# Kernel optimization log

Measured on AMD Instinct MI355X. Metric: run time of the kernel, lower is better.

Reference implementation:

```python
import jax, jax.numpy as jnp
import numpy as np

B, S, D = 2, 2048, 1024
H = 16
HEAD_DIM = 64          # matches head_dim init arg; D // H == 64
HALF_WINDOW = 32       # local_window_size // 2
SCALE = HEAD_DIM ** -0.5


def setup_inputs() -> dict:
    key = jax.random.key(0)
    ks = jax.random.split(key, 6)
    std = 1.0 / np.sqrt(D)
    return {
        "x": jax.random.normal(ks[0], (B, S, D), dtype=jnp.float32),
        "Wq": jax.random.normal(ks[1], (D, D), dtype=jnp.float32) * std,
        "Wk": jax.random.normal(ks[2], (D, D), dtype=jnp.float32) * std,
        "Wv": jax.random.normal(ks[3], (D, D), dtype=jnp.float32) * std,
        "Wo": jax.random.normal(ks[4], (D, D), dtype=jnp.float32) * std,
        "bo": jnp.zeros((D,), dtype=jnp.float32),
    }


def reference(x, Wq, Wk, Wv, Wo, bo):
    b, s, d = x.shape
    h, hd = H, d // H

    def split_heads(y):  # [b, s, d] -> [b, h, s, hd]
        return y.reshape(b, s, h, hd).transpose(0, 2, 1, 3)

    q = split_heads(x @ Wq) * SCALE
    k = split_heads(x @ Wk)
    v = split_heads(x @ Wv)

    # dense scores [b, h, s, s] (module materializes full O(S^2) matrix)
    scores = jnp.einsum("bhqd,bhkd->bhqk", q, k)

    # local window |i-j| <= HALF_WINDOW combined with causal j <= i
    i = jnp.arange(s)
    local = jnp.abs(i[:, None] - i[None, :]) <= HALF_WINDOW
    causal = i[None, :] <= i[:, None]
    mask = local & causal  # [s, s]
    scores = jnp.where(mask[None, None, :, :], scores, -jnp.inf)

    attn = jax.nn.softmax(scores, axis=-1)  # diagonal always valid -> no NaN
    out = jnp.einsum("bhqk,bhkd->bhqd", attn, v)
    out = out.transpose(0, 2, 1, 3).reshape(b, s, d)  # merge heads
    return out @ Wo + bo
```

## Files before the change

### kernel.cpp

```cpp
#include <hip/hip_runtime.h>
#include <hip/hip_bf16.h>

typedef __bf16 bf16_t;
typedef __bf16 bf16x8 __attribute__((ext_vector_type(8)));
typedef __bf16 bf16x4 __attribute__((ext_vector_type(4)));
typedef float  f32x4  __attribute__((ext_vector_type(4)));

#define B_   2
#define S_   2048
#define D_   1024
#define H_   16
#define HD_  64
#define HW   32
#define SCALE_ 0.125f

__device__ __forceinline__ void gl_lds16(const bf16_t* g, bf16_t* l) {
  __builtin_amdgcn_global_load_lds(
      (const __attribute__((address_space(1))) void*)g,
      (__attribute__((address_space(3))) void*)l, 16, 0, 0);
}

__global__ __launch_bounds__(256) void k_conv(const float* __restrict__ X,
                                              const float* __restrict__ W0,
                                              const float* __restrict__ W1,
                                              const float* __restrict__ W2,
                                              const float* __restrict__ W3,
                                              bf16_t* __restrict__ Xb,
                                              bf16_t* __restrict__ Wt) {
  __shared__ bf16_t t[64][72];
  int bid = blockIdx.x;
  int tid = threadIdx.x;
  if (bid < 2048) {
    int i = bid * 256 + tid;
    const float4 a = ((const float4*)X)[i * 2];
    const float4 b = ((const float4*)X)[i * 2 + 1];
    bf16x8 r;
    r[0] = (bf16_t)a.x; r[1] = (bf16_t)a.y; r[2] = (bf16_t)a.z; r[3] = (bf16_t)a.w;
    r[4] = (bf16_t)b.x; r[5] = (bf16_t)b.y; r[6] = (bf16_t)b.z; r[7] = (bf16_t)b.w;
    ((bf16x8*)Xb)[i] = r;
    return;
  }
  int wb = bid - 2048;
  int wsel = wb >> 8;
  const float* W = (wsel == 0) ? W0 : (wsel == 1) ? W1 : (wsel == 2) ? W2 : W3;
  bf16_t* dst = Wt + (size_t)wsel * D_ * D_;
  int tile = wb & 255;
  int k0 = (tile >> 4) * 64, n0 = (tile & 15) * 64;
  int r = tid >> 4, c4 = (tid & 15) * 4;
#pragma unroll
  for (int i = 0; i < 4; ++i) {
    int row = i * 16 + r;
    float4 v = *(const float4*)(W + (size_t)(k0 + row) * D_ + n0 + c4);
    t[row][c4 + 0] = (bf16_t)v.x;
    t[row][c4 + 1] = (bf16_t)v.y;
    t[row][c4 + 2] = (bf16_t)v.z;
    t[row][c4 + 3] = (bf16_t)v.w;
  }
  __syncthreads();
#pragma unroll
  for (int i = 0; i < 4; ++i) {
    int row = i * 16 + r;
    bf16x4 o;
    o[0] = t[c4 + 0][row];
    o[1] = t[c4 + 1][row];
    o[2] = t[c4 + 2][row];
    o[3] = t[c4 + 3][row];
    *(bf16x4*)(dst + (size_t)(n0 + row) * D_ + k0 + c4) = o;
  }
}

__global__ __launch_bounds__(256) void k_gemm_qkv(const bf16_t* __restrict__ X,
                                                  const bf16_t* __restrict__ Wt,
                                                  bf16_t* __restrict__ Q,
                                                  bf16_t* __restrict__ K,
                                                  bf16_t* __restrict__ V) {
  __shared__ bf16_t sA[128 * 32];
  __shared__ bf16_t sB[128 * 32];
  int bid = blockIdx.x;
  int xcd = bid & 7, idx = bid >> 3;
  int mt = ((xcd & 3) << 3) + (idx & 7);
  int nt = (xcd >> 2) * 12 + (idx >> 3);
  int wsel = nt >> 3;
  int n0 = (nt & 7) * 128, m0 = mt * 128;
  const bf16_t* Wp = Wt + (size_t)wsel * D_ * D_;
  int tid = threadIdx.x, lane = tid & 63, wave = tid >> 6;
  int wr = (wave >> 1) * 64, wc = (wave & 1) * 64;
  int r0 = wave * 32 + (lane >> 2);
  int ce = (lane & 3) * 8;
  const bf16_t* gA0 = X + (size_t)(m0 + r0) * D_ + ce;
  const bf16_t* gB0 = Wp + (size_t)(n0 + r0) * D_ + ce;
  bf16_t* lA0 = sA + wave * 1024;
  bf16_t* lB0 = sB + wave * 1024;
  f32x4 acc[4][4] = {};
  int kq = (lane >> 4) * 8, rl = lane & 15;
  for (int kt = 0; kt < D_; kt += 32) {
    __syncthreads();
    gl_lds16(gA0 + kt, lA0);
    gl_lds16(gA0 + kt + (size_t)16 * D_, lA0 + 512);
    gl_lds16(gB0 + kt, lB0);
    gl_lds16(gB0 + kt + (size_t)16 * D_, lB0 + 512);
    __syncthreads();
    bf16x8 af[4], bfr[4];
#pragma unroll
    for (int m = 0; m < 4; ++m)
      af[m] = *(const bf16x8*)&sA[(wr + m * 16 + rl) * 32 + kq];
#pragma unroll
    for (int n = 0; n < 4; ++n)
      bfr[n] = *(const bf16x8*)&sB[(wc + n * 16 + rl) * 32 + kq];
#pragma unroll
    for (int m = 0; m < 4; ++m)
#pragma unroll
      for (int n = 0; n < 4; ++n)
        acc[m][n] = __builtin_amdgcn_mfma_f32_16x16x32_bf16(af[m], bfr[n], acc[m][n], 0, 0, 0);
  }
  float qscale = (wsel == 0) ? SCALE_ : 1.0f;
#pragma unroll
  for (int m = 0; m < 4; ++m) {
#pragma unroll
    for (int n = 0; n < 4; ++n) {
#pragma unroll
      for (int r = 0; r < 4; ++r) {
        int gm = m0 + wr + m * 16 + (lane >> 4) * 4 + r;
        int gn = n0 + wc + n * 16 + rl;
        int b = gm >> 11, s = gm & 2047;
        int h = gn >> 6, hd = gn & 63;
        bf16_t val = (bf16_t)(acc[m][n][r] * qscale);
        if (wsel == 0)
          Q[(((size_t)(b * H_ + h)) * S_ + s) * HD_ + hd] = val;
        else if (wsel == 1)
          K[(((size_t)(b * H_ + h)) * S_ + s) * HD_ + hd] = val;
        else
          V[(((size_t)(b * H_ + h)) * HD_ + hd) * S_ + s] = val;
      }
    }
  }
}

__global__ __launch_bounds__(256) void k_gemm_out(const bf16_t* __restrict__ A,
                                                  const bf16_t* __restrict__ Wp,
                                                  const float* __restrict__ bo,
                                                  float* __restrict__ out) {
  __shared__ bf16_t sA[128 * 32];
  __shared__ bf16_t sB[128 * 32];
  int bid = blockIdx.x;
  int xcd = bid & 7, idx = bid >> 3;
  int mt = ((xcd & 3) << 3) + (idx & 7);
  int nt = ((xcd >> 2) << 2) + (idx >> 3);
  int n0 = nt * 128, m0 = mt * 128;
  int tid = threadIdx.x, lane = tid & 63, wave = tid >> 6;
  int wr = (wave >> 1) * 64, wc = (wave & 1) * 64;
  int r0 = wave * 32 + (lane >> 2);
  int ce = (lane & 3) * 8;
  const bf16_t* gA0 = A + (size_t)(m0 + r0) * D_ + ce;
  const bf16_t* gB0 = Wp + (size_t)(n0 + r0) * D_ + ce;
  bf16_t* lA0 = sA + wave * 1024;
  bf16_t* lB0 = sB + wave * 1024;
  f32x4 acc[4][4] = {};
  int kq = (lane >> 4) * 8, rl = lane & 15;
  for (int kt = 0; kt < D_; kt += 32) {
    __syncthreads();
    gl_lds16(gA0 + kt, lA0);
    gl_lds16(gA0 + kt + (size_t)16 * D_, lA0 + 512);
    gl_lds16(gB0 + kt, lB0);
    gl_lds16(gB0 + kt + (size_t)16 * D_, lB0 + 512);
    __syncthreads();
    bf16x8 af[4], bfr[4];
#pragma unroll
    for (int m = 0; m < 4; ++m)
      af[m] = *(const bf16x8*)&sA[(wr + m * 16 + rl) * 32 + kq];
#pragma unroll
    for (int n = 0; n < 4; ++n)
      bfr[n] = *(const bf16x8*)&sB[(wc + n * 16 + rl) * 32 + kq];
#pragma unroll
    for (int m = 0; m < 4; ++m)
#pragma unroll
      for (int n = 0; n < 4; ++n)
        acc[m][n] = __builtin_amdgcn_mfma_f32_16x16x32_bf16(af[m], bfr[n], acc[m][n], 0, 0, 0);
  }
#pragma unroll
  for (int m = 0; m < 4; ++m) {
#pragma unroll
    for (int n = 0; n < 4; ++n) {
#pragma unroll
      for (int r = 0; r < 4; ++r) {
        int gm = m0 + wr + m * 16 + (lane >> 4) * 4 + r;
        int gn = n0 + wc + n * 16 + rl;
        out[(size_t)gm * D_ + gn] = acc[m][n][r] + bo[gn];
      }
    }
  }
}

#define QB 64
#define KW 112
#define KLP 72
#define VTP 120

__global__ __launch_bounds__(256) void k_attn(const bf16_t* __restrict__ Q,
                                              const bf16_t* __restrict__ K,
                                              const bf16_t* __restrict__ Vt,
                                              bf16_t* __restrict__ O) {
  __shared__ bf16_t sK[KW][KLP];
  __shared__ bf16_t sV[HD_][VTP];
  __shared__ bf16_t sQ[QB][KLP];
  __shared__ bf16_t sP[4][16][KLP];
  int bid = blockIdx.x;
  int qb = bid & 31, bh = bid >> 5;
  int q0 = qb * QB;
  const bf16_t* Kp = K + (size_t)bh * S_ * HD_;
  const bf16_t* Vp = Vt + (size_t)bh * HD_ * S_;
  const bf16_t* Qp = Q + (size_t)bh * S_ * HD_;
  int tid = threadIdx.x;
  int wk0b = q0 - HW;
  for (int idx = tid; idx < KW * 8; idx += 256) {
    int row = idx >> 3, c8 = (idx & 7) * 8;
    int kg = wk0b + row;
    kg = kg < 0 ? 0 : (kg > S_ - 1 ? S_ - 1 : kg);
    *(bf16x8*)&sK[row][c8] = *(const bf16x8*)(Kp + (size_t)kg * HD_ + c8);
  }
  for (int idx = tid; idx < HD_ * 14; idx += 256) {
    int row = idx / 14, c8 = (idx % 14) * 8;
    int ks = wk0b + c8;
    ks = ks < 0 ? 0 : (ks > S_ - 8 ? S_ - 8 : ks);
    *(bf16x8*)&sV[row][c8] = *(const bf16x8*)(Vp + (size_t)row * S_ + ks);
  }
  for (int idx = tid; idx < QB * 8; idx += 256) {
    int row = idx >> 3, c8 = (idx & 7) * 8;
    *(bf16x8*)&sQ[row][c8] = *(const bf16x8*)(Qp + (size_t)(q0 + row) * HD_ + c8);
  }
  __syncthreads();
  int lane = tid & 63, wave = tid >> 6;
  int rl = lane & 15, hi = lane >> 4;
  int wko = wave * 16;
  f32x4 accs[4] = {};
#pragma unroll
  for (int ds = 0; ds < 2; ++ds) {
    bf16x8 qf = *(const bf16x8*)&sQ[wave * 16 + rl][ds * 32 + hi * 8];
#pragma unroll
    for (int kb = 0; kb < 4; ++kb) {
      bf16x8 kf = *(const bf16x8*)&sK[wko + kb * 16 + rl][ds * 32 + hi * 8];
      accs[kb] = __builtin_amdgcn_mfma_f32_16x16x32_bf16(kf, qf, accs[kb], 0, 0, 0);
    }
  }
  float p[4][4];
  float mx = -1e30f;
#pragma unroll
  for (int kb = 0; kb < 4; ++kb) {
#pragma unroll
    for (int r = 0; r < 4; ++r) {
      int kl = kb * 16 + hi * 4 + r;
      bool valid = (kl >= rl) && (kl <= rl + HW) && (wk0b + wko + kl >= 0);
      float s = valid ? accs[kb][r] : -1e30f;
      p[kb][r] = s;
      mx = fmaxf(mx, s);
    }
  }
  mx = fmaxf(mx, __shfl_xor(mx, 16));
  mx = fmaxf(mx, __shfl_xor(mx, 32));
  float sum = 0.f;
#pragma unroll
  for (int kb = 0; kb < 4; ++kb)
#pragma unroll
    for (int r = 0; r < 4; ++r) {
      p[kb][r] = __expf(p[kb][r] - mx);
      sum += p[kb][r];
    }
  sum += __shfl_xor(sum, 16);
  sum += __shfl_xor(sum, 32);
  float inv = 1.f / sum;
#pragma unroll
  for (int kb = 0; kb < 4; ++kb) {
    bf16x4 pv;
#pragma unroll
    for (int r = 0; r < 4; ++r) pv[r] = (bf16_t)(p[kb][r] * inv);
    *(bf16x4*)&sP[wave][rl][kb * 16 + hi * 4] = pv;
  }
  f32x4 acco[4] = {};
#pragma unroll
  for (int ks = 0; ks < 2; ++ks) {
    bf16x8 aP = *(const bf16x8*)&sP[wave][rl][ks * 32 + hi * 8];
#pragma unroll
    for (int n = 0; n < 4; ++n) {
      bf16x8 bV = *(const bf16x8*)&sV[n * 16 + rl][wko + ks * 32 + hi * 8];
      acco[n] = __builtin_amdgcn_mfma_f32_16x16x32_bf16(aP, bV, acco[n], 0, 0, 0);
    }
  }
  int b = bh >> 4, h = bh & 15;
#pragma unroll
  for (int n = 0; n < 4; ++n) {
#pragma unroll
    for (int r = 0; r < 4; ++r) {
      int qgl = q0 + wave * 16 + hi * 4 + r;
      int d = n * 16 + rl;
      O[((size_t)(b * S_ + qgl)) * D_ + h * HD_ + d] = (bf16_t)acco[n][r];
    }
  }
}

extern "C" void kernel_launch(void* const* d_in, const int* in_sizes, int n_in,
                              void* d_out, int out_size, void* d_ws, size_t ws_size,
                              hipStream_t stream) {
  const float* x  = (const float*)d_in[0];
  const float* Wq = (const float*)d_in[1];
  const float* Wk = (const float*)d_in[2];
  const float* Wv = (const float*)d_in[3];
  const float* Wo = (const float*)d_in[4];
  const float* bo = (const float*)d_in[5];
  float* out = (float*)d_out;
  char* ws = (char*)d_ws;
  bf16_t* xb = (bf16_t*)(ws);
  bf16_t* wt = (bf16_t*)(ws + (size_t)(8 << 20));
  bf16_t* qb = (bf16_t*)(ws + (size_t)(16 << 20));
  bf16_t* kb = (bf16_t*)(ws + (size_t)(24 << 20));
  bf16_t* vb = (bf16_t*)(ws + (size_t)(32 << 20));
  bf16_t* ob = (bf16_t*)(ws + (size_t)(40 << 20));

  hipLaunchKernelGGL(k_conv, dim3(3072), dim3(256), 0, stream,
                     x, Wq, Wk, Wv, Wo, xb, wt);
  hipLaunchKernelGGL(k_gemm_qkv, dim3(768), dim3(256), 0, stream, xb, wt, qb, kb, vb);
  hipLaunchKernelGGL(k_attn, dim3(1024), dim3(256), 0, stream, qb, kb, vb, ob);
  hipLaunchKernelGGL(k_gemm_out, dim3(256), dim3(256), 0, stream,
                     ob, wt + (size_t)3 * D_ * D_, bo, out);
}
```

Baseline: 91.43 us.

## Widen GEMM K-tile to 64 with XOR-swizzled LDS and drop XCD block remap

Both the QKV and output projection GEMMs now stage 64-wide K slices per iteration instead of 32, which halves the number of barrier pairs per tile. The LDS layout uses an XOR swizzle on 16-byte chunks so that the MFMA fragment reads avoid bank conflicts. The XCD-aware block-to-tile remapping is replaced by a plain mt/nt decomposition. LDS use per block doubles to 32KB, and the simpler mapping may reduce L2 locality across XCDs.

```diff
diff --git a/kernel.cpp b/kernel.cpp
--- a/kernel.cpp
+++ b/kernel.cpp
@@ -74,44 +74,48 @@
                                                   bf16_t* __restrict__ Q,
                                                   bf16_t* __restrict__ K,
                                                   bf16_t* __restrict__ V) {
-  __shared__ bf16_t sA[128 * 32];
-  __shared__ bf16_t sB[128 * 32];
+  __shared__ bf16_t sA[128 * 64];
+  __shared__ bf16_t sB[128 * 64];
   int bid = blockIdx.x;
-  int xcd = bid & 7, idx = bid >> 3;
-  int mt = ((xcd & 3) << 3) + (idx & 7);
-  int nt = (xcd >> 2) * 12 + (idx >> 3);
+  int mt = bid & 31, nt = bid >> 5;
   int wsel = nt >> 3;
   int n0 = (nt & 7) * 128, m0 = mt * 128;
   const bf16_t* Wp = Wt + (size_t)wsel * D_ * D_;
   int tid = threadIdx.x, lane = tid & 63, wave = tid >> 6;
   int wr = (wave >> 1) * 64, wc = (wave & 1) * 64;
-  int r0 = wave * 32 + (lane >> 2);
-  int ce = (lane & 3) * 8;
-  const bf16_t* gA0 = X + (size_t)(m0 + r0) * D_ + ce;
-  const bf16_t* gB0 = Wp + (size_t)(n0 + r0) * D_ + ce;
-  bf16_t* lA0 = sA + wave * 1024;
-  bf16_t* lB0 = sB + wave * 1024;
+  int srow = lane >> 3;
+  int scol = ((lane & 7) ^ srow) * 8;
+  const bf16_t* gA0 = X + (size_t)(m0 + wave * 32 + srow) * D_ + scol;
+  const bf16_t* gB0 = Wp + (size_t)(n0 + wave * 32 + srow) * D_ + scol;
+  bf16_t* lA0 = sA + wave * 2048;
+  bf16_t* lB0 = sB + wave * 2048;
   f32x4 acc[4][4] = {};
-  int kq = (lane >> 4) * 8, rl = lane & 15;
-  for (int kt = 0; kt < D_; kt += 32) {
+  int rl = lane & 15, hi = lane >> 4;
+  int r7 = rl & 7;
+  for (int kt = 0; kt < D_; kt += 64) {
     __syncthreads();
-    gl_lds16(gA0 + kt, lA0);
-    gl_lds16(gA0 + kt + (size_t)16 * D_, lA0 + 512);
-    gl_lds16(gB0 + kt, lB0);
-    gl_lds16(gB0 + kt + (size_t)16 * D_, lB0 + 512);
+#pragma unroll
+    for (int i = 0; i < 4; ++i) {
+      gl_lds16(gA0 + kt + (size_t)(i * 8) * D_, lA0 + i * 512);
+      gl_lds16(gB0 + kt + (size_t)(i * 8) * D_, lB0 + i * 512);
+    }
     __syncthreads();
-    bf16x8 af[4], bfr[4];
-#pragma unroll
-    for (int m = 0; m < 4; ++m)
-      af[m] = *(const bf16x8*)&sA[(wr + m * 16 + rl) * 32 + kq];
-#pragma unroll
-    for (int n = 0; n < 4; ++n)
-      bfr[n] = *(const bf16x8*)&sB[(wc + n * 16 + rl) * 32 + kq];
-#pragma unroll
-    for (int m = 0; m < 4; ++m)
+#pragma unroll
+    for (int kk = 0; kk < 2; ++kk) {
+      int cofs = (((kk * 4 + hi) ^ r7)) * 8;
+      bf16x8 af[4], bfr[4];
+#pragma unroll
+      for (int m = 0; m < 4; ++m)
+        af[m] = *(const bf16x8*)&sA[(wr + m * 16 + rl) * 64 + cofs];
 #pragma unroll
       for (int n = 0; n < 4; ++n)
-        acc[m][n] = __builtin_amdgcn_mfma_f32_16x16x32_bf16(af[m], bfr[n], acc[m][n], 0, 0, 0);
+        bfr[n] = *(const bf16x8*)&sB[(wc + n * 16 + rl) * 64 + cofs];
+#pragma unroll
+      for (int m = 0; m < 4; ++m)
+#pragma unroll
+        for (int n = 0; n < 4; ++n)
+          acc[m][n] = __builtin_amdgcn_mfma_f32_16x16x32_bf16(af[m], bfr[n], acc[m][n], 0, 0, 0);
+    }
   }
   float qscale = (wsel == 0) ? SCALE_ : 1.0f;
 #pragma unroll
@@ -120,7 +124,7 @@
     for (int n = 0; n < 4; ++n) {
 #pragma unroll
       for (int r = 0; r < 4; ++r) {
-        int gm = m0 + wr + m * 16 + (lane >> 4) * 4 + r;
+        int gm = m0 + wr + m * 16 + hi * 4 + r;
         int gn = n0 + wc + n * 16 + rl;
         int b = gm >> 11, s = gm & 2047;
         int h = gn >> 6, hd = gn & 63;
@@ -140,42 +144,46 @@
                                                   const bf16_t* __restrict__ Wp,
                                                   const float* __restrict__ bo,
                                                   float* __restrict__ out) {
-  __shared__ bf16_t sA[128 * 32];
-  __shared__ bf16_t sB[128 * 32];
+  __shared__ bf16_t sA[128 * 64];
+  __shared__ bf16_t sB[128 * 64];
   int bid = blockIdx.x;
-  int xcd = bid & 7, idx = bid >> 3;
-  int mt = ((xcd & 3) << 3) + (idx & 7);
-  int nt = ((xcd >> 2) << 2) + (idx >> 3);
+  int mt = bid & 31, nt = bid >> 5;
   int n0 = nt * 128, m0 = mt * 128;
   int tid = threadIdx.x, lane = tid & 63, wave = tid >> 6;
   int wr = (wave >> 1) * 64, wc = (wave & 1) * 64;
-  int r0 = wave * 32 + (lane >> 2);
-  int ce = (lane & 3) * 8;
-  const bf16_t* gA0 = A + (size_t)(m0 + r0) * D_ + ce;
-  const bf16_t* gB0 = Wp + (size_t)(n0 + r0) * D_ + ce;
-  bf16_t* lA0 = sA + wave * 1024;
-  bf16_t* lB0 = sB + wave * 1024;
+  int srow = lane >> 3;
+  int scol = ((lane & 7) ^ srow) * 8;
+  const bf16_t* gA0 = A + (size_t)(m0 + wave * 32 + srow) * D_ + scol;
+  const bf16_t* gB0 = Wp + (size_t)(n0 + wave * 32 + srow) * D_ + scol;
+  bf16_t* lA0 = sA + wave * 2048;
+  bf16_t* lB0 = sB + wave * 2048;
   f32x4 acc[4][4] = {};
-  int kq = (lane >> 4) * 8, rl = lane & 15;
-  for (int kt = 0; kt < D_; kt += 32) {
+  int rl = lane & 15, hi = lane >> 4;
+  int r7 = rl & 7;
+  for (int kt = 0; kt < D_; kt += 64) {
     __syncthreads();
-    gl_lds16(gA0 + kt, lA0);
-    gl_lds16(gA0 + kt + (size_t)16 * D_, lA0 + 512);
-    gl_lds16(gB0 + kt, lB0);
-    gl_lds16(gB0 + kt + (size_t)16 * D_, lB0 + 512);
+#pragma unroll
+    for (int i = 0; i < 4; ++i) {
+      gl_lds16(gA0 + kt + (size_t)(i * 8) * D_, lA0 + i * 512);
+      gl_lds16(gB0 + kt + (size_t)(i * 8) * D_, lB0 + i * 512);
+    }
     __syncthreads();
-    bf16x8 af[4], bfr[4];
-#pragma unroll
-    for (int m = 0; m < 4; ++m)
-      af[m] = *(const bf16x8*)&sA[(wr + m * 16 + rl) * 32 + kq];
-#pragma unroll
-    for (int n = 0; n < 4; ++n)
-      bfr[n] = *(const bf16x8*)&sB[(wc + n * 16 + rl) * 32 + kq];
-#pragma unroll
-    for (int m = 0; m < 4; ++m)
+#pragma unroll
+    for (int kk = 0; kk < 2; ++kk) {
+      int cofs = (((kk * 4 + hi) ^ r7)) * 8;
+      bf16x8 af[4], bfr[4];
+#pragma unroll
+      for (int m = 0; m < 4; ++m)
+        af[m] = *(const bf16x8*)&sA[(wr + m * 16 + rl) * 64 + cofs];
 #pragma unroll
       for (int n = 0; n < 4; ++n)
-        acc[m][n] = __builtin_amdgcn_mfma_f32_16x16x32_bf16(af[m], bfr[n], acc[m][n], 0, 0, 0);
+        bfr[n] = *(const bf16x8*)&sB[(wc + n * 16 + rl) * 64 + cofs];
+#pragma unroll
+      for (int m = 0; m < 4; ++m)
+#pragma unroll
+        for (int n = 0; n < 4; ++n)
+          acc[m][n] = __builtin_amdgcn_mfma_f32_16x16x32_bf16(af[m], bfr[n], acc[m][n], 0, 0, 0);
+    }
   }
 #pragma unroll
   for (int m = 0; m < 4; ++m) {
@@ -183,7 +191,7 @@
     for (int n = 0; n < 4; ++n) {
 #pragma unroll
       for (int r = 0; r < 4; ++r) {
-        int gm = m0 + wr + m * 16 + (lane >> 4) * 4 + r;
+        int gm = m0 + wr + m * 16 + hi * 4 + r;
         int gn = n0 + wc + n * 16 + rl;
         out[(size_t)gm * D_ + gn] = acc[m][n][r] + bo[gn];
       }
```

Measured after the change: 90.00 us. About the same (-1.6%).

## Shrink GEMM tiles to 64x128, drop XCD swizzle, load Q fragments directly in attention

Applied to the files above, without the earlier changes.

Both GEMMs move from 128x128 to 64x128 block tiles with 32-column per-wave slices, doubling the grid (1536 and 512 blocks) so more CUs are busy on MI355X. The XCD-aware block swizzle is replaced by a simple row-major mapping. The attention kernel loads Q fragments straight from global into registers, dropping the sQ LDS staging, and shrinks LDS row padding. Smaller tiles lower arithmetic intensity and L2 reuse, and the new padding may change LDS bank conflicts.

```diff
diff --git a/kernel.cpp b/kernel.cpp
--- a/kernel.cpp
+++ b/kernel.cpp
@@ -74,53 +74,63 @@
                                                   bf16_t* __restrict__ Q,
                                                   bf16_t* __restrict__ K,
                                                   bf16_t* __restrict__ V) {
-  __shared__ bf16_t sA[128 * 32];
+  __shared__ bf16_t sA[64 * 32];
   __shared__ bf16_t sB[128 * 32];
   int bid = blockIdx.x;
-  int xcd = bid & 7, idx = bid >> 3;
-  int mt = ((xcd & 3) << 3) + (idx & 7);
-  int nt = (xcd >> 2) * 12 + (idx >> 3);
+  int mt = bid & 63, nt = bid >> 6;
   int wsel = nt >> 3;
-  int n0 = (nt & 7) * 128, m0 = mt * 128;
+  int n0 = (nt & 7) * 128, m0 = mt * 64;
   const bf16_t* Wp = Wt + (size_t)wsel * D_ * D_;
   int tid = threadIdx.x, lane = tid & 63, wave = tid >> 6;
-  int wr = (wave >> 1) * 64, wc = (wave & 1) * 64;
-  int r0 = wave * 32 + (lane >> 2);
-  int ce = (lane & 3) * 8;
-  const bf16_t* gA0 = X + (size_t)(m0 + r0) * D_ + ce;
-  const bf16_t* gB0 = Wp + (size_t)(n0 + r0) * D_ + ce;
-  bf16_t* lA0 = sA + wave * 1024;
-  bf16_t* lB0 = sB + wave * 1024;
-  f32x4 acc[4][4] = {};
-  int kq = (lane >> 4) * 8, rl = lane & 15;
+  int wc = wave * 32;
+  int crow = lane >> 2, ccol = (lane & 3) * 8;
+  const bf16_t* gsrc0; bf16_t* ldst0;
+  const bf16_t* gsrc1; bf16_t* ldst1;
+  const bf16_t* gsrc2; bf16_t* ldst2;
+#pragma unroll
+  for (int j = 0; j < 3; ++j) {
+    int c = wave * 3 + j;
+    const bf16_t* g; bf16_t* l;
+    if (c < 4) {
+      g = X + (size_t)(m0 + c * 16 + crow) * D_ + ccol;
+      l = sA + c * 512;
+    } else {
+      g = Wp + (size_t)(n0 + (c - 4) * 16 + crow) * D_ + ccol;
+      l = sB + (c - 4) * 512;
+    }
+    if (j == 0) { gsrc0 = g; ldst0 = l; }
+    else if (j == 1) { gsrc1 = g; ldst1 = l; }
+    else { gsrc2 = g; ldst2 = l; }
+  }
+  f32x4 acc[4][2] = {};
+  int kq = (lane >> 4) * 8, rl = lane & 15, hi = lane >> 4;
   for (int kt = 0; kt < D_; kt += 32) {
     __syncthreads();
-    gl_lds16(gA0 + kt, lA0);
-    gl_lds16(gA0 + kt + (size_t)16 * D_, lA0 + 512);
-    gl_lds16(gB0 + kt, lB0);
-    gl_lds16(gB0 + kt + (size_t)16 * D_, lB0 + 512);
+    gl_lds16(gsrc0 + kt, ldst0);
+    gl_lds16(gsrc1 + kt, ldst1);
+    gl_lds16(gsrc2 + kt, ldst2);
     __syncthreads();
-    bf16x8 af[4], bfr[4];
+    bf16x8 af[4], bfr[2];
 #pragma unroll
     for (int m = 0; m < 4; ++m)
-      af[m] = *(const bf16x8*)&sA[(wr + m * 16 + rl) * 32 + kq];
-#pragma unroll
-    for (int n = 0; n < 4; ++n)
+      af[m] = *(const bf16x8*)&sA[(m * 16 + rl) * 32 + kq];
+#pragma unroll
+    for (int n = 0; n < 2; ++n)
       bfr[n] = *(const bf16x8*)&sB[(wc + n * 16 + rl) * 32 + kq];
 #pragma unroll
     for (int m = 0; m < 4; ++m)
 #pragma unroll
-      for (int n = 0; n < 4; ++n)
+      for (int n = 0; n < 2; ++n)
         acc[m][n] = __builtin_amdgcn_mfma_f32_16x16x32_bf16(af[m], bfr[n], acc[m][n], 0, 0, 0);
   }
   float qscale = (wsel == 0) ? SCALE_ : 1.0f;
 #pragma unroll
   for (int m = 0; m < 4; ++m) {
 #pragma unroll
-    for (int n = 0; n < 4; ++n) {
+    for (int n = 0; n < 2; ++n) {
 #pragma unroll
       for (int r = 0; r < 4; ++r) {
-        int gm = m0 + wr + m * 16 + (lane >> 4) * 4 + r;
+        int gm = m0 + m * 16 + hi * 4 + r;
         int gn = n0 + wc + n * 16 + rl;
         int b = gm >> 11, s = gm & 2047;
         int h = gn >> 6, hd = gn & 63;
@@ -140,50 +150,60 @@
                                                   const bf16_t* __restrict__ Wp,
                                                   const float* __restrict__ bo,
                                                   float* __restrict__ out) {
-  __shared__ bf16_t sA[128 * 32];
+  __shared__ bf16_t sA[64 * 32];
   __shared__ bf16_t sB[128 * 32];
   int bid = blockIdx.x;
-  int xcd = bid & 7, idx = bid >> 3;
-  int mt = ((xcd & 3) << 3) + (idx & 7);
-  int nt = ((xcd >> 2) << 2) + (idx >> 3);
-  int n0 = nt * 128, m0 = mt * 128;
+  int mt = bid & 63, nt = bid >> 6;
+  int n0 = nt * 128, m0 = mt * 64;
   int tid = threadIdx.x, lane = tid & 63, wave = tid >> 6;
-  int wr = (wave >> 1) * 64, wc = (wave & 1) * 64;
-  int r0 = wave * 32 + (lane >> 2);
-  int ce = (lane & 3) * 8;
-  const bf16_t* gA0 = A + (size_t)(m0 + r0) * D_ + ce;
-  const bf16_t* gB0 = Wp + (size_t)(n0 + r0) * D_ + ce;
-  bf16_t* lA0 = sA + wave * 1024;
-  bf16_t* lB0 = sB + wave * 1024;
-  f32x4 acc[4][4] = {};
-  int kq = (lane >> 4) * 8, rl = lane & 15;
+  int wc = wave * 32;
+  int crow = lane >> 2, ccol = (lane & 3) * 8;
+  const bf16_t* gsrc0; bf16_t* ldst0;
+  const bf16_t* gsrc1; bf16_t* ldst1;
+  const bf16_t* gsrc2; bf16_t* ldst2;
+#pragma unroll
+  for (int j = 0; j < 3; ++j) {
+    int c = wave * 3 + j;
+    const bf16_t* g; bf16_t* l;
+    if (c < 4) {
+      g = A + (size_t)(m0 + c * 16 + crow) * D_ + ccol;
+      l = sA + c * 512;
+    } else {
+      g = Wp + (size_t)(n0 + (c - 4) * 16 + crow) * D_ + ccol;
+      l = sB + (c - 4) * 512;
+    }
+    if (j == 0) { gsrc0 = g; ldst0 = l; }
+    else if (j == 1) { gsrc1 = g; ldst1 = l; }
+    else { gsrc2 = g; ldst2 = l; }
+  }
+  f32x4 acc[4][2] = {};
+  int kq = (lane >> 4) * 8, rl = lane & 15, hi = lane >> 4;
   for (int kt = 0; kt < D_; kt += 32) {
     __syncthreads();
-    gl_lds16(gA0 + kt, lA0);
-    gl_lds16(gA0 + kt + (size_t)16 * D_, lA0 + 512);
-    gl_lds16(gB0 + kt, lB0);
-    gl_lds16(gB0 + kt + (size_t)16 * D_, lB0 + 512);
+    gl_lds16(gsrc0 + kt, ldst0);
+    gl_lds16(gsrc1 + kt, ldst1);
+    gl_lds16(gsrc2 + kt, ldst2);
     __syncthreads();
-    bf16x8 af[4], bfr[4];
+    bf16x8 af[4], bfr[2];
 #pragma unroll
     for (int m = 0; m < 4; ++m)
-      af[m] = *(const bf16x8*)&sA[(wr + m * 16 + rl) * 32 + kq];
-#pragma unroll
-    for (int n = 0; n < 4; ++n)
+      af[m] = *(const bf16x8*)&sA[(m * 16 + rl) * 32 + kq];
+#pragma unroll
+    for (int n = 0; n < 2; ++n)
       bfr[n] = *(const bf16x8*)&sB[(wc + n * 16 + rl) * 32 + kq];
 #pragma unroll
     for (int m = 0; m < 4; ++m)
 #pragma unroll
-      for (int n = 0; n < 4; ++n)
+      for (int n = 0; n < 2; ++n)
         acc[m][n] = __builtin_amdgcn_mfma_f32_16x16x32_bf16(af[m], bfr[n], acc[m][n], 0, 0, 0);
   }
 #pragma unroll
   for (int m = 0; m < 4; ++m) {
 #pragma unroll
-    for (int n = 0; n < 4; ++n) {
+    for (int n = 0; n < 2; ++n) {
 #pragma unroll
       for (int r = 0; r < 4; ++r) {
-        int gm = m0 + wr + m * 16 + (lane >> 4) * 4 + r;
+        int gm = m0 + m * 16 + hi * 4 + r;
         int gn = n0 + wc + n * 16 + rl;
         out[(size_t)gm * D_ + gn] = acc[m][n][r] + bo[gn];
       }
@@ -193,8 +213,8 @@
 
 #define QB 64
 #define KW 112
-#define KLP 72
-#define VTP 120
+#define KLP 68
+#define VTP 116
 
 __global__ __launch_bounds__(256) void k_attn(const bf16_t* __restrict__ Q,
                                               const bf16_t* __restrict__ K,
@@ -202,7 +222,6 @@
                                               bf16_t* __restrict__ O) {
   __shared__ bf16_t sK[KW][KLP];
   __shared__ bf16_t sV[HD_][VTP];
-  __shared__ bf16_t sQ[QB][KLP];
   __shared__ bf16_t sP[4][16][KLP];
   int bid = blockIdx.x;
   int qb = bid & 31, bh = bid >> 5;
@@ -211,7 +230,11 @@
   const bf16_t* Vp = Vt + (size_t)bh * HD_ * S_;
   const bf16_t* Qp = Q + (size_t)bh * S_ * HD_;
   int tid = threadIdx.x;
+  int lane = tid & 63, wave = tid >> 6;
+  int rl = lane & 15, hi = lane >> 4;
   int wk0b = q0 - HW;
+  bf16x8 qf0 = *(const bf16x8*)(Qp + (size_t)(q0 + wave * 16 + rl) * HD_ + hi * 8);
+  bf16x8 qf1 = *(const bf16x8*)(Qp + (size_t)(q0 + wave * 16 + rl) * HD_ + 32 + hi * 8);
   for (int idx = tid; idx < KW * 8; idx += 256) {
     int row = idx >> 3, c8 = (idx & 7) * 8;
     int kg = wk0b + row;
@@ -224,23 +247,18 @@
     ks = ks < 0 ? 0 : (ks > S_ - 8 ? S_ - 8 : ks);
     *(bf16x8*)&sV[row][c8] = *(const bf16x8*)(Vp + (size_t)row * S_ + ks);
   }
-  for (int idx = tid; idx < QB * 8; idx += 256) {
-    int row = idx >> 3, c8 = (idx & 7) * 8;
-    *(bf16x8*)&sQ[row][c8] = *(const bf16x8*)(Qp + (size_t)(q0 + row) * HD_ + c8);
-  }
   __syncthreads();
-  int lane = tid & 63, wave = tid >> 6;
-  int rl = lane & 15, hi = lane >> 4;
   int wko = wave * 16;
   f32x4 accs[4] = {};
 #pragma unroll
-  for (int ds = 0; ds < 2; ++ds) {
-    bf16x8 qf = *(const bf16x8*)&sQ[wave * 16 + rl][ds * 32 + hi * 8];
-#pragma unroll
-    for (int kb = 0; kb < 4; ++kb) {
-      bf16x8 kf = *(const bf16x8*)&sK[wko + kb * 16 + rl][ds * 32 + hi * 8];
-      accs[kb] = __builtin_amdgcn_mfma_f32_16x16x32_bf16(kf, qf, accs[kb], 0, 0, 0);
-    }
+  for (int kb = 0; kb < 4; ++kb) {
+    bf16x8 kf = *(const bf16x8*)&sK[wko + kb * 16 + rl][hi * 8];
+    accs[kb] = __builtin_amdgcn_mfma_f32_16x16x32_bf16(kf, qf0, accs[kb], 0, 0, 0);
+  }
+#pragma unroll
+  for (int kb = 0; kb < 4; ++kb) {
+    bf16x8 kf = *(const bf16x8*)&sK[wko + kb * 16 + rl][32 + hi * 8];
+    accs[kb] = __builtin_amdgcn_mfma_f32_16x16x32_bf16(kf, qf1, accs[kb], 0, 0, 0);
   }
   float p[4][4];
   float mx = -1e30f;
@@ -317,8 +335,8 @@
 
   hipLaunchKernelGGL(k_conv, dim3(3072), dim3(256), 0, stream,
                      x, Wq, Wk, Wv, Wo, xb, wt);
-  hipLaunchKernelGGL(k_gemm_qkv, dim3(768), dim3(256), 0, stream, xb, wt, qb, kb, vb);
+  hipLaunchKernelGGL(k_gemm_qkv, dim3(1536), dim3(256), 0, stream, xb, wt, qb, kb, vb);
   hipLaunchKernelGGL(k_attn, dim3(1024), dim3(256), 0, stream, qb, kb, vb, ob);
-  hipLaunchKernelGGL(k_gemm_out, dim3(256), dim3(256), 0, stream,
+  hipLaunchKernelGGL(k_gemm_out, dim3(512), dim3(256), 0, stream,
                      ob, wt + (size_t)3 * D_ * D_, bo, out);
 }
```

After: 99.13 us. 8.4% more time.
